# Optimization experiments

Hardware: AMD Instinct MI355X
Metric: run time of the kernel (lower is better)

Reference implementation:

```python
import jax, jax.numpy as jnp
import numpy as np

H = 16   # nheads
WIN = 64 # window_size (= sqrt(n) so the b,h,n//w,n//w,dk view is valid)


def setup_inputs() -> dict:
    key = jax.random.key(0)
    ks = jax.random.split(key, 7)
    b, n, d = 4, 4096, 1024
    q = jax.random.normal(ks[0], (b, n, d), dtype=jnp.float32)
    k = jax.random.normal(ks[1], (b, n, d), dtype=jnp.float32)
    v = jax.random.normal(ks[2], (b, n, d), dtype=jnp.float32)
    # nn.Linear(d, d, bias=False) weights, stored torch-style as (out, in)
    Wq = jax.random.normal(ks[3], (d, d), dtype=jnp.float32) * 0.02
    Wk = jax.random.normal(ks[4], (d, d), dtype=jnp.float32) * 0.02
    Wv = jax.random.normal(ks[5], (d, d), dtype=jnp.float32) * 0.02
    Wo = jax.random.normal(ks[6], (d, d), dtype=jnp.float32) * 0.02
    return {"q": q, "k": k, "v": v, "Wq": Wq, "Wk": Wk, "Wv": Wv, "Wo": Wo, "window": 1}


def _attention(q, k, v, Wq, Wk, Wv, Wo, window):
    b, qn, d = q.shape
    n = k.shape[1]
    dk = d // H
    # torch Linear: x @ W.T
    qh = (q @ Wq.T).reshape(b, qn, H, dk).transpose(0, 2, 1, 3)  # (b,h,qn,dk)
    kh = (k @ Wk.T).reshape(b, n, H, dk).transpose(0, 2, 1, 3)
    vh = (v @ Wv.T).reshape(b, n, H, dk).transpose(0, 2, 1, 3)
    if window and WIN > 0:
        nw = n // WIN  # requires n == nw*nw, as in the torch .view
        qh = qh.reshape(b, H, nw, nw, dk)
        kh = kh.reshape(b, H, nw, nw, dk)
        vh = vh.reshape(b, H, nw, nw, dk)
    scale = jnp.float32(1.0) / jnp.sqrt(jnp.float32(dk))
    attn = jnp.einsum('...qd,...kd->...qk', qh, kh) * scale  # block-local scores
    attn = jax.nn.softmax(attn, axis=-1)
    o = jnp.einsum('...qk,...kd->...qd', attn, vh)
    # torch: attn.transpose(1, -2).contiguous().view(b, qn, d)
    o = jnp.swapaxes(o, 1, -2).reshape(b, qn, d)
    return o @ Wo.T


def reference(q, k, v, Wq, Wk, Wv, Wo, window):
    return _attention(q, k, v, Wq, Wk, Wv, Wo, window)
```

## Files before the change

kernel.cpp:

```cpp
#include <hip/hip_runtime.h>


typedef unsigned short u16;
typedef unsigned int u32;
typedef __bf16 bf16x8 __attribute__((ext_vector_type(8)));
typedef float f32x4 __attribute__((ext_vector_type(4)));
typedef u16 u16x8 __attribute__((ext_vector_type(8)));

__device__ __forceinline__ u16 f2bf(float f) {
  u32 u = __builtin_bit_cast(u32, f);
  u += 0x7fffu + ((u >> 16) & 1u);
  return (u16)(u >> 16);
}

__device__ __forceinline__ u16x8 cvt2(float4 a, float4 b) {
  u16x8 r;
  r[0] = f2bf(a.x); r[1] = f2bf(a.y); r[2] = f2bf(a.z); r[3] = f2bf(a.w);
  r[4] = f2bf(b.x); r[5] = f2bf(b.y); r[6] = f2bf(b.z); r[7] = f2bf(b.w);
  return r;
}

__global__ __launch_bounds__(256) void cvtw3_kernel(
    const float* __restrict__ Wq, const float* __restrict__ Wk,
    const float* __restrict__ Wv, u16* __restrict__ dst) {
  const float* src = (blockIdx.z == 0) ? Wq : (blockIdx.z == 1) ? Wk : Wv;
  const size_t i = ((size_t)blockIdx.x * 256 + threadIdx.x) * 8;
  const float4 a = *(const float4*)(src + i);
  const float4 b = *(const float4*)(src + i + 4);
  *(u16x8*)(dst + (size_t)blockIdx.z * 1048576 + i) = cvt2(a, b);
}

__device__ __forceinline__ void cp16(const u16* g, u16* l) {
  __builtin_amdgcn_global_load_lds((const __attribute__((address_space(1))) void*)g,
                                   (__attribute__((address_space(3))) void*)l, 16, 0, 0);
}

template <int AF32, int BF32, int CF32>
__global__ __launch_bounds__(256, 2) void gemm_t_kernel(
    const void* __restrict__ Av, const void* __restrict__ Bv,
    void* __restrict__ Cv) {
  constexpr int N = 1024, K = 1024;
  __shared__ u16 lA[2][128 * 32];
  __shared__ u16 lB[2][128 * 32];
  const int tid = threadIdx.x;
  const int lane = tid & 63, w = tid >> 6;
  const int quad = lane >> 4, lr = lane & 15;
  const int lid = blockIdx.x;
  const int xcd = lid & 7, slot = lid >> 3;
  const int m0 = (xcd * 16 + (slot >> 3)) * 128;
  const int n0 = (slot & 7) * 128;
  const int wr = (w >> 1) * 64, wc = (w & 1) * 64;

  const int ch1 = tid, ch2 = tid + 256;

  const u16* A16 = (const u16*)Av;
  const float* A32 = (const float*)Av;
  const u16* B16 = (const u16*)Bv;
  const float* B32 = (const float*)Bv;

  const u16* Ag1 = A16 + (size_t)(m0 + (ch1 >> 2)) * K + (ch1 & 3) * 8;
  const u16* Ag2 = A16 + (size_t)(m0 + (ch2 >> 2)) * K + (ch2 & 3) * 8;
  const u16* Bg1 = B16 + (size_t)(n0 + (ch1 >> 2)) * K + (ch1 & 3) * 8;
  const u16* Bg2 = B16 + (size_t)(n0 + (ch2 >> 2)) * K + (ch2 & 3) * 8;
  const float* Af1 = A32 + (size_t)(m0 + (ch1 >> 2)) * K + (ch1 & 3) * 8;
  const float* Af2 = A32 + (size_t)(m0 + (ch2 >> 2)) * K + (ch2 & 3) * 8;
  const float* Bf1 = B32 + (size_t)(n0 + (ch1 >> 2)) * K + (ch1 & 3) * 8;
  const float* Bf2 = B32 + (size_t)(n0 + (ch2 >> 2)) * K + (ch2 & 3) * 8;

  float4 fA0, fA1, fA2, fA3, fB0, fB1, fB2, fB3;

  if constexpr (AF32) {
    fA0 = *(const float4*)(Af1);     fA1 = *(const float4*)(Af1 + 4);
    fA2 = *(const float4*)(Af2);     fA3 = *(const float4*)(Af2 + 4);
    *(u16x8*)&lA[0][ch1 * 8] = cvt2(fA0, fA1);
    *(u16x8*)&lA[0][ch2 * 8] = cvt2(fA2, fA3);
  } else {
    cp16(Ag1, &lA[0][ch1 * 8]);
    cp16(Ag2, &lA[0][ch2 * 8]);
  }
  if constexpr (BF32) {
    fB0 = *(const float4*)(Bf1);     fB1 = *(const float4*)(Bf1 + 4);
    fB2 = *(const float4*)(Bf2);     fB3 = *(const float4*)(Bf2 + 4);
    *(u16x8*)&lB[0][ch1 * 8] = cvt2(fB0, fB1);
    *(u16x8*)&lB[0][ch2 * 8] = cvt2(fB2, fB3);
  } else {
    cp16(Bg1, &lB[0][ch1 * 8]);
    cp16(Bg2, &lB[0][ch2 * 8]);
  }
  __syncthreads();

  f32x4 acc[4][4] = {};
#pragma unroll 1
  for (int t = 0; t < 32; ++t) {
    const int cur = t & 1, nxt = cur ^ 1;
    const int k1 = (t + 1) * 32;
    const bool more = (t < 31);
    if (more) {
      if constexpr (AF32) {
        fA0 = *(const float4*)(Af1 + k1); fA1 = *(const float4*)(Af1 + k1 + 4);
        fA2 = *(const float4*)(Af2 + k1); fA3 = *(const float4*)(Af2 + k1 + 4);
      } else {
        cp16(Ag1 + k1, &lA[nxt][ch1 * 8]);
        cp16(Ag2 + k1, &lA[nxt][ch2 * 8]);
      }
      if constexpr (BF32) {
        fB0 = *(const float4*)(Bf1 + k1); fB1 = *(const float4*)(Bf1 + k1 + 4);
        fB2 = *(const float4*)(Bf2 + k1); fB3 = *(const float4*)(Bf2 + k1 + 4);
      } else {
        cp16(Bg1 + k1, &lB[nxt][ch1 * 8]);
        cp16(Bg2 + k1, &lB[nxt][ch2 * 8]);
      }
    }
    bf16x8 afr[4], bfr[4];
#pragma unroll
    for (int mi = 0; mi < 4; ++mi)
      afr[mi] = *(const bf16x8*)&lA[cur][(wr + mi * 16 + lr) * 32 + quad * 8];
#pragma unroll
    for (int ni = 0; ni < 4; ++ni)
      bfr[ni] = *(const bf16x8*)&lB[cur][(wc + ni * 16 + lr) * 32 + quad * 8];
#pragma unroll
    for (int mi = 0; mi < 4; ++mi)
#pragma unroll
      for (int ni = 0; ni < 4; ++ni)
        acc[mi][ni] = __builtin_amdgcn_mfma_f32_16x16x32_bf16(
            afr[mi], bfr[ni], acc[mi][ni], 0, 0, 0);
    if (more) {
      if constexpr (AF32) {
        *(u16x8*)&lA[nxt][ch1 * 8] = cvt2(fA0, fA1);
        *(u16x8*)&lA[nxt][ch2 * 8] = cvt2(fA2, fA3);
      }
      if constexpr (BF32) {
        *(u16x8*)&lB[nxt][ch1 * 8] = cvt2(fB0, fB1);
        *(u16x8*)&lB[nxt][ch2 * 8] = cvt2(fB2, fB3);
      }
    }
    __syncthreads();
  }

#pragma unroll
  for (int mi = 0; mi < 4; ++mi)
#pragma unroll
    for (int r = 0; r < 4; ++r) {
      const int row = m0 + wr + mi * 16 + quad * 4 + r;
      if constexpr (!CF32) {
        u16* dst = (u16*)Cv + (size_t)row * N + n0 + wc + lr;
#pragma unroll
        for (int ni = 0; ni < 4; ++ni) dst[ni * 16] = f2bf(acc[mi][ni][r]);
      } else {
        float* dst = (float*)Cv + (size_t)row * N + n0 + wc + lr;
#pragma unroll
        for (int ni = 0; ni < 4; ++ni) dst[ni * 16] = acc[mi][ni][r];
      }
    }
}

__global__ __launch_bounds__(64) void attn_win_kernel(
    const u16* __restrict__ Xq, const u16* __restrict__ Xk, const u16* __restrict__ Xv,
    u16* __restrict__ Xo) {
  __shared__ u16 P[64 * 72];
  const int bx = blockIdx.x;
  const int wi = bx & 63, h = (bx >> 6) & 15, b = bx >> 10;
  const int lane = threadIdx.x & 63, quad = lane >> 4, lr = lane & 15;
  const size_t tb = (size_t)b * 4096 + wi * 64;
  const u16* qb = Xq + tb * 1024 + h * 64;
  const u16* kb = Xk + tb * 1024 + h * 64;
  const u16* vb = Xv + tb * 1024 + h * 64;

  bf16x8 aq[4][2], bk[4][2];
#pragma unroll
  for (int mi = 0; mi < 4; ++mi)
#pragma unroll
    for (int ks = 0; ks < 2; ++ks) {
      aq[mi][ks] = *(const bf16x8*)(qb + (size_t)(mi * 16 + lr) * 1024 + ks * 32 + quad * 8);
      bk[mi][ks] = *(const bf16x8*)(kb + (size_t)(mi * 16 + lr) * 1024 + ks * 32 + quad * 8);
    }
  f32x4 s[4][4];
#pragma unroll
  for (int mi = 0; mi < 4; ++mi)
#pragma unroll
    for (int ni = 0; ni < 4; ++ni) {
      f32x4 z = {0.f, 0.f, 0.f, 0.f};
      z = __builtin_amdgcn_mfma_f32_16x16x32_bf16(aq[mi][0], bk[ni][0], z, 0, 0, 0);
      s[mi][ni] = __builtin_amdgcn_mfma_f32_16x16x32_bf16(aq[mi][1], bk[ni][1], z, 0, 0, 0);
    }

  u16x8 bvr[2][4];
#pragma unroll
  for (int ks = 0; ks < 2; ++ks)
#pragma unroll
    for (int ci = 0; ci < 4; ++ci) {
      const u16* vc = vb + (size_t)(ks * 32 + quad * 8) * 1024 + ci * 16 + lr;
#pragma unroll
      for (int j = 0; j < 8; ++j) bvr[ks][ci][j] = vc[(size_t)j * 1024];
    }

  const float sc = 0.125f;
#pragma unroll
  for (int mi = 0; mi < 4; ++mi)
#pragma unroll
    for (int r = 0; r < 4; ++r) {
      float mx = fmaxf(fmaxf(s[mi][0][r], s[mi][1][r]), fmaxf(s[mi][2][r], s[mi][3][r]));
#pragma unroll
      for (int m = 1; m < 16; m <<= 1) mx = fmaxf(mx, __shfl_xor(mx, m));
      float sum = 0.f;
#pragma unroll
      for (int ni = 0; ni < 4; ++ni) {
        float p = __expf((s[mi][ni][r] - mx) * sc);
        s[mi][ni][r] = p;
        sum += p;
      }
#pragma unroll
      for (int m = 1; m < 16; m <<= 1) sum += __shfl_xor(sum, m);
      const float inv = 1.f / sum;
#pragma unroll
      for (int ni = 0; ni < 4; ++ni) s[mi][ni][r] *= inv;
    }

#pragma unroll
  for (int mi = 0; mi < 4; ++mi)
#pragma unroll
    for (int ni = 0; ni < 4; ++ni)
#pragma unroll
      for (int r = 0; r < 4; ++r)
        P[(mi * 16 + quad * 4 + r) * 72 + ni * 16 + lr] = f2bf(s[mi][ni][r]);
  __syncthreads();

  f32x4 o[4][4] = {};
#pragma unroll
  for (int ks = 0; ks < 2; ++ks) {
    bf16x8 ap[4];
#pragma unroll
    for (int mi = 0; mi < 4; ++mi)
      ap[mi] = *(const bf16x8*)&P[(mi * 16 + lr) * 72 + ks * 32 + quad * 8];
#pragma unroll
    for (int mi = 0; mi < 4; ++mi)
#pragma unroll
      for (int ci = 0; ci < 4; ++ci)
        o[mi][ci] = __builtin_amdgcn_mfma_f32_16x16x32_bf16(
            ap[mi], __builtin_bit_cast(bf16x8, bvr[ks][ci]), o[mi][ci], 0, 0, 0);
  }

#pragma unroll
  for (int mi = 0; mi < 4; ++mi)
#pragma unroll
    for (int r = 0; r < 4; ++r) {
      const int qp = mi * 16 + quad * 4 + r;
      u16* dst = Xo + ((size_t)b * 4096 + (size_t)qp * 64 + wi) * 1024 + h * 64 + lr;
#pragma unroll
      for (int ci = 0; ci < 4; ++ci) dst[ci * 16] = f2bf(o[mi][ci][r]);
    }
}

extern "C" void kernel_launch(void* const* d_in, const int* in_sizes, int n_in,
                              void* d_out, int out_size, void* d_ws, size_t ws_size,
                              hipStream_t stream) {
  (void)in_sizes; (void)n_in; (void)out_size; (void)ws_size;
  const float* q  = (const float*)d_in[0];
  const float* k  = (const float*)d_in[1];
  const float* v  = (const float*)d_in[2];
  const float* Wq = (const float*)d_in[3];
  const float* Wk = (const float*)d_in[4];
  const float* Wv = (const float*)d_in[5];
  const float* Wo = (const float*)d_in[6];

  constexpr size_t ELEMS = (size_t)16384 * 1024;
  u16* Xq  = (u16*)d_out;
  u16* Wb3 = (u16*)d_out + ELEMS;
  u16* Xo  = (u16*)d_ws;
  u16* Xk  = Xo + ELEMS;
  u16* Xv  = Xk + ELEMS;

  cvtw3_kernel<<<dim3(512, 1, 3), 256, 0, stream>>>(Wq, Wk, Wv, Wb3);
  gemm_t_kernel<1, 0, 0><<<1024, 256, 0, stream>>>(q, Wb3,           Xq);
  gemm_t_kernel<1, 0, 0><<<1024, 256, 0, stream>>>(k, Wb3 + 1048576, Xk);
  gemm_t_kernel<1, 0, 0><<<1024, 256, 0, stream>>>(v, Wb3 + 2097152, Xv);
  attn_win_kernel<<<dim3(4096), 64, 0, stream>>>(Xq, Xk, Xv, Xo);
  gemm_t_kernel<0, 1, 1><<<1024, 256, 0, stream>>>(Xo, Wo, (float*)d_out);
}
```

Before: 489.0 us.

## Stage fp32 GEMM operands via direct global-to-LDS loads with swizzle, convert at fragment load

Reworks the GEMM so fp32 operands are copied straight into LDS with global_load_lds, using an XOR swizzle, instead of passing through registers. They are converted to bf16 only when MFMA fragments are read, which removes register staging and the separate store of converted tiles. The double buffer is dropped in favour of a single buffer loaded at the top of each k-step with two barriers, so loads no longer overlap with MFMA work. This risks exposing memory latency, and the fp32 tiles double the LDS footprint for the A side.

```diff
diff --git a/kernel.cpp b/kernel.cpp
--- a/kernel.cpp
+++ b/kernel.cpp
@@ -30,18 +30,20 @@
   *(u16x8*)(dst + (size_t)blockIdx.z * 1048576 + i) = cvt2(a, b);
 }
 
-__device__ __forceinline__ void cp16(const u16* g, u16* l) {
+__device__ __forceinline__ void cp16(const void* g, void* l) {
   __builtin_amdgcn_global_load_lds((const __attribute__((address_space(1))) void*)g,
                                    (__attribute__((address_space(3))) void*)l, 16, 0, 0);
 }
 
-template <int AF32, int BF32, int CF32>
-__global__ __launch_bounds__(256, 2) void gemm_t_kernel(
+template <int AF, int BF, int CF>
+__global__ __launch_bounds__(256, 2) void gemm_m_kernel(
     const void* __restrict__ Av, const void* __restrict__ Bv,
     void* __restrict__ Cv) {
   constexpr int N = 1024, K = 1024;
-  __shared__ u16 lA[2][128 * 32];
-  __shared__ u16 lB[2][128 * 32];
+  __shared__ u16  lA16[AF ? 8 : 128 * 32];
+  __shared__ float lA32[AF ? 128 * 32 : 8];
+  __shared__ u16  lB16[BF ? 8 : 128 * 32];
+  __shared__ float lB32[BF ? 128 * 32 : 8];
   const int tid = threadIdx.x;
   const int lane = tid & 63, w = tid >> 6;
   const int quad = lane >> 4, lr = lane & 15;
@@ -51,89 +53,96 @@
   const int n0 = (slot & 7) * 128;
   const int wr = (w >> 1) * 64, wc = (w & 1) * 64;
 
+  const u16* A16 = (const u16*)Av; const float* A32 = (const float*)Av;
+  const u16* B16 = (const u16*)Bv; const float* B32 = (const float*)Bv;
+
   const int ch1 = tid, ch2 = tid + 256;
-
-  const u16* A16 = (const u16*)Av;
-  const float* A32 = (const float*)Av;
-  const u16* B16 = (const u16*)Bv;
-  const float* B32 = (const float*)Bv;
-
-  const u16* Ag1 = A16 + (size_t)(m0 + (ch1 >> 2)) * K + (ch1 & 3) * 8;
-  const u16* Ag2 = A16 + (size_t)(m0 + (ch2 >> 2)) * K + (ch2 & 3) * 8;
-  const u16* Bg1 = B16 + (size_t)(n0 + (ch1 >> 2)) * K + (ch1 & 3) * 8;
-  const u16* Bg2 = B16 + (size_t)(n0 + (ch2 >> 2)) * K + (ch2 & 3) * 8;
-  const float* Af1 = A32 + (size_t)(m0 + (ch1 >> 2)) * K + (ch1 & 3) * 8;
-  const float* Af2 = A32 + (size_t)(m0 + (ch2 >> 2)) * K + (ch2 & 3) * 8;
-  const float* Bf1 = B32 + (size_t)(n0 + (ch1 >> 2)) * K + (ch1 & 3) * 8;
-  const float* Bf2 = B32 + (size_t)(n0 + (ch2 >> 2)) * K + (ch2 & 3) * 8;
-
-  float4 fA0, fA1, fA2, fA3, fB0, fB1, fB2, fB3;
-
-  if constexpr (AF32) {
-    fA0 = *(const float4*)(Af1);     fA1 = *(const float4*)(Af1 + 4);
-    fA2 = *(const float4*)(Af2);     fA3 = *(const float4*)(Af2 + 4);
-    *(u16x8*)&lA[0][ch1 * 8] = cvt2(fA0, fA1);
-    *(u16x8*)&lA[0][ch2 * 8] = cvt2(fA2, fA3);
+  const u16 *Ag1 = nullptr, *Ag2 = nullptr, *Bg1 = nullptr, *Bg2 = nullptr;
+  const float *Afp[4], *Bfp[4];
+  if constexpr (!AF) {
+    Ag1 = A16 + (size_t)(m0 + (ch1 >> 2)) * K + (ch1 & 3) * 8;
+    Ag2 = A16 + (size_t)(m0 + (ch2 >> 2)) * K + (ch2 & 3) * 8;
   } else {
-    cp16(Ag1, &lA[0][ch1 * 8]);
-    cp16(Ag2, &lA[0][ch2 * 8]);
-  }
-  if constexpr (BF32) {
-    fB0 = *(const float4*)(Bf1);     fB1 = *(const float4*)(Bf1 + 4);
-    fB2 = *(const float4*)(Bf2);     fB3 = *(const float4*)(Bf2 + 4);
-    *(u16x8*)&lB[0][ch1 * 8] = cvt2(fB0, fB1);
-    *(u16x8*)&lB[0][ch2 * 8] = cvt2(fB2, fB3);
+#pragma unroll
+    for (int i = 0; i < 4; ++i) {
+      const int s = tid + 256 * i, row = s >> 3, gp = s & 7;
+      Afp[i] = A32 + (size_t)(m0 + row) * K + ((gp ^ (row & 7)) << 2);
+    }
+  }
+  if constexpr (!BF) {
+    Bg1 = B16 + (size_t)(n0 + (ch1 >> 2)) * K + (ch1 & 3) * 8;
+    Bg2 = B16 + (size_t)(n0 + (ch2 >> 2)) * K + (ch2 & 3) * 8;
   } else {
-    cp16(Bg1, &lB[0][ch1 * 8]);
-    cp16(Bg2, &lB[0][ch2 * 8]);
-  }
-  __syncthreads();
+#pragma unroll
+    for (int i = 0; i < 4; ++i) {
+      const int s = tid + 256 * i, row = s >> 3, gp = s & 7;
+      Bfp[i] = B32 + (size_t)(n0 + row) * K + ((gp ^ (row & 7)) << 2);
+    }
+  }
 
   f32x4 acc[4][4] = {};
 #pragma unroll 1
   for (int t = 0; t < 32; ++t) {
-    const int cur = t & 1, nxt = cur ^ 1;
-    const int k1 = (t + 1) * 32;
-    const bool more = (t < 31);
-    if (more) {
-      if constexpr (AF32) {
-        fA0 = *(const float4*)(Af1 + k1); fA1 = *(const float4*)(Af1 + k1 + 4);
-        fA2 = *(const float4*)(Af2 + k1); fA3 = *(const float4*)(Af2 + k1 + 4);
-      } else {
-        cp16(Ag1 + k1, &lA[nxt][ch1 * 8]);
-        cp16(Ag2 + k1, &lA[nxt][ch2 * 8]);
-      }
-      if constexpr (BF32) {
-        fB0 = *(const float4*)(Bf1 + k1); fB1 = *(const float4*)(Bf1 + k1 + 4);
-        fB2 = *(const float4*)(Bf2 + k1); fB3 = *(const float4*)(Bf2 + k1 + 4);
-      } else {
-        cp16(Bg1 + k1, &lB[nxt][ch1 * 8]);
-        cp16(Bg2 + k1, &lB[nxt][ch2 * 8]);
-      }
-    }
+    const int k0 = t * 32;
+    if constexpr (!AF) {
+      cp16(Ag1 + k0, &lA16[ch1 * 8]);
+      cp16(Ag2 + k0, &lA16[ch2 * 8]);
+    } else {
+#pragma unroll
+      for (int i = 0; i < 4; ++i) cp16(Afp[i] + k0, &lA32[(tid + 256 * i) * 4]);
+    }
+    if constexpr (!BF) {
+      cp16(Bg1 + k0, &lB16[ch1 * 8]);
+      cp16(Bg2 + k0, &lB16[ch2 * 8]);
+    } else {
+#pragma unroll
+      for (int i = 0; i < 4; ++i) cp16(Bfp[i] + k0, &lB32[(tid + 256 * i) * 4]);
+    }
+    __syncthreads();
+
     bf16x8 afr[4], bfr[4];
-#pragma unroll
-    for (int mi = 0; mi < 4; ++mi)
-      afr[mi] = *(const bf16x8*)&lA[cur][(wr + mi * 16 + lr) * 32 + quad * 8];
-#pragma unroll
-    for (int ni = 0; ni < 4; ++ni)
-      bfr[ni] = *(const bf16x8*)&lB[cur][(wc + ni * 16 + lr) * 32 + quad * 8];
+    if constexpr (!AF) {
+#pragma unroll
+      for (int mi = 0; mi < 4; ++mi)
+        afr[mi] = *(const bf16x8*)&lA16[(wr + mi * 16 + lr) * 32 + quad * 8];
+    } else {
+#pragma unroll
+      for (int mi = 0; mi < 4; ++mi) {
+        const int row = wr + mi * 16 + lr;
+        const int g1 = (2 * quad) ^ (row & 7);
+        const f32x4 x0 = *(const f32x4*)&lA32[row * 32 + g1 * 4];
+        const f32x4 x1 = *(const f32x4*)&lA32[row * 32 + (g1 ^ 1) * 4];
+#pragma unroll
+        for (int j = 0; j < 4; ++j) {
+          afr[mi][j] = (__bf16)x0[j];
+          afr[mi][j + 4] = (__bf16)x1[j];
+        }
+      }
+    }
+    if constexpr (!BF) {
+#pragma unroll
+      for (int ni = 0; ni < 4; ++ni)
+        bfr[ni] = *(const bf16x8*)&lB16[(wc + ni * 16 + lr) * 32 + quad * 8];
+    } else {
+#pragma unroll
+      for (int ni = 0; ni < 4; ++ni) {
+        const int row = wc + ni * 16 + lr;
+        const int g1 = (2 * quad) ^ (row & 7);
+        const f32x4 x0 = *(const f32x4*)&lB32[row * 32 + g1 * 4];
+        const f32x4 x1 = *(const f32x4*)&lB32[row * 32 + (g1 ^ 1) * 4];
+#pragma unroll
+        for (int j = 0; j < 4; ++j) {
+          bfr[ni][j] = (__bf16)x0[j];
+          bfr[ni][j + 4] = (__bf16)x1[j];
+        }
+      }
+    }
 #pragma unroll
     for (int mi = 0; mi < 4; ++mi)
 #pragma unroll
       for (int ni = 0; ni < 4; ++ni)
         acc[mi][ni] = __builtin_amdgcn_mfma_f32_16x16x32_bf16(
             afr[mi], bfr[ni], acc[mi][ni], 0, 0, 0);
-    if (more) {
-      if constexpr (AF32) {
-        *(u16x8*)&lA[nxt][ch1 * 8] = cvt2(fA0, fA1);
-        *(u16x8*)&lA[nxt][ch2 * 8] = cvt2(fA2, fA3);
-      }
-      if constexpr (BF32) {
-        *(u16x8*)&lB[nxt][ch1 * 8] = cvt2(fB0, fB1);
-        *(u16x8*)&lB[nxt][ch2 * 8] = cvt2(fB2, fB3);
-      }
-    }
     __syncthreads();
   }
 
@@ -142,7 +151,7 @@
 #pragma unroll
     for (int r = 0; r < 4; ++r) {
       const int row = m0 + wr + mi * 16 + quad * 4 + r;
-      if constexpr (!CF32) {
+      if constexpr (!CF) {
         u16* dst = (u16*)Cv + (size_t)row * N + n0 + wc + lr;
 #pragma unroll
         for (int ni = 0; ni < 4; ++ni) dst[ni * 16] = f2bf(acc[mi][ni][r]);
@@ -266,14 +275,14 @@
   constexpr size_t ELEMS = (size_t)16384 * 1024;
   u16* Xq  = (u16*)d_out;
   u16* Wb3 = (u16*)d_out + ELEMS;
-  u16* Xo  = (u16*)d_ws;
-  u16* Xk  = Xo + ELEMS;
+  u16* Xk  = (u16*)d_ws;
   u16* Xv  = Xk + ELEMS;
+  u16* Xo  = Xv + ELEMS;
 
   cvtw3_kernel<<<dim3(512, 1, 3), 256, 0, stream>>>(Wq, Wk, Wv, Wb3);
-  gemm_t_kernel<1, 0, 0><<<1024, 256, 0, stream>>>(q, Wb3,           Xq);
-  gemm_t_kernel<1, 0, 0><<<1024, 256, 0, stream>>>(k, Wb3 + 1048576, Xk);
-  gemm_t_kernel<1, 0, 0><<<1024, 256, 0, stream>>>(v, Wb3 + 2097152, Xv);
+  gemm_m_kernel<1, 0, 0><<<1024, 256, 0, stream>>>(q, Wb3,           Xq);
+  gemm_m_kernel<1, 0, 0><<<1024, 256, 0, stream>>>(k, Wb3 + 1048576, Xk);
+  gemm_m_kernel<1, 0, 0><<<1024, 256, 0, stream>>>(v, Wb3 + 2097152, Xv);
   attn_win_kernel<<<dim3(4096), 64, 0, stream>>>(Xq, Xk, Xv, Xo);
-  gemm_t_kernel<0, 1, 1><<<1024, 256, 0, stream>>>(Xo, Wo, (float*)d_out);
-}
+  gemm_m_kernel<0, 1, 1><<<1024, 256, 0, stream>>>(Xo, Wo, (float*)d_out);
+}
```

Measured after the change: 492.7 us. About the same (+0.8%).
